# Optimization experiments

Hardware: AMD Instinct MI355X
Metric: run time of the kernel (lower is better)

## Reference

```python
import jax, jax.numpy as jnp
import numpy as np

B, T, J, C = 32, 256, 21, 3
BT = B * T
N = BT * J

_TPL_SRC = np.array([0, 1, 2, 3, 4, 0, 5, 6, 7, 8, 0, 9, 10, 11, 12, 0, 13, 14, 15, 16, 0, 17, 18, 19, 20], np.int32)
_TPL_DST = np.array([1, 2, 3, 4, 0, 5, 6, 7, 8, 0, 9, 10, 11, 12, 0, 13, 14, 15, 16, 0, 17, 18, 19, 20, 0], np.int32)


def _build_edges():
    off = (np.arange(BT, dtype=np.int32) * J)[:, None]
    src = (_TPL_SRC[None, :] + off).ravel()
    dst = (_TPL_DST[None, :] + off).ravel()
    # PyG GATConv default add_self_loops=True (both layers see the same augmented set)
    loops = np.arange(N, dtype=np.int32)
    return np.concatenate([src, loops]), np.concatenate([dst, loops])


def setup_inputs() -> dict:
    key = jax.random.key(0)
    ks = jax.random.split(key, 8)
    src, dst = _build_edges()
    return {
        "keypoints": jax.random.normal(ks[0], (B, T, J, C), jnp.float32),
        "W1": jax.random.normal(ks[1], (3, 256), jnp.float32) * 0.3,
        "att1_src": jax.random.normal(ks[2], (4, 64), jnp.float32) * 0.1,
        "att1_dst": jax.random.normal(ks[3], (4, 64), jnp.float32) * 0.1,
        "b1": jnp.zeros((256,), jnp.float32),
        "W2": jax.random.normal(ks[4], (256, 128), jnp.float32) * 0.06,
        "att2_src": jax.random.normal(ks[5], (1, 128), jnp.float32) * 0.1,
        "att2_dst": jax.random.normal(ks[6], (1, 128), jnp.float32) * 0.1,
        "b2": jnp.zeros((128,), jnp.float32),
        "src": jnp.asarray(src),
        "dst": jnp.asarray(dst),
    }


def _gat_conv(x, src, dst, W, a_src, a_dst, b, heads, d_head):
    n = x.shape[0]
    h = (x @ W).reshape(n, heads, d_head)            # [N,H,D]
    e_s = jnp.einsum('nhd,hd->nh', h, a_src)          # [N,H]
    e_d = jnp.einsum('nhd,hd->nh', h, a_dst)
    e = jax.nn.leaky_relu(e_s[src] + e_d[dst], 0.2)   # [E,H]
    m = jax.ops.segment_max(e, dst, num_segments=n)
    ex = jnp.exp(e - m[dst])
    z = jax.ops.segment_sum(ex, dst, num_segments=n)
    alpha = ex / z[dst]                               # scatter-softmax over dst
    out = jax.ops.segment_sum(h[src] * alpha[:, :, None], dst, num_segments=n)
    return out.reshape(n, heads * d_head) + b


def reference(keypoints, W1, att1_src, att1_dst, b1, W2, att2_src, att2_dst, b2, src, dst):
    x = keypoints.reshape(N, C)
    x = jax.nn.relu(_gat_conv(x, src, dst, W1, att1_src, att1_dst, b1, 4, 64))
    x = jax.nn.relu(_gat_conv(x, src, dst, W2, att2_src, att2_dst, b2, 1, 128))
    x = x.reshape(BT, J, 128).mean(axis=1)            # pool joints
    return x.reshape(B, T, 128).mean(axis=1)          # pool time -> [B,128]
```

## Files before the change

kernel.cpp:

```cpp
#include <hip/hip_runtime.h>

#define NJ  21
#define X1S 264
#define H2S 136
#define XAS 40

typedef __attribute__((ext_vector_type(8))) short  bf16x8;
typedef __attribute__((ext_vector_type(4))) float  floatx4;

__device__ __forceinline__ float lrelu(float v){ return v > 0.f ? v : 0.2f*v; }
__device__ __forceinline__ unsigned short f2bf(float x){
  unsigned int u = __float_as_uint(x);
  return (unsigned short)((u + 0x7FFFu + ((u >> 16) & 1u)) >> 16);
}
__device__ __forceinline__ float bf2f(unsigned short h){
  return __uint_as_float(((unsigned int)h) << 16);
}

__global__ void prep(const float* __restrict__ W1, const float* __restrict__ a1s,
                     const float* __restrict__ a1d, const float* __restrict__ W2,
                     unsigned short* __restrict__ w2f, unsigned short* __restrict__ w1b,
                     float* __restrict__ ws1o){
  const int t = threadIdx.x, b = blockIdx.x;
  if (b < 32){
    int base = b*1024 + t*4;
    #pragma unroll
    for (int i = 0; i < 4; ++i){
      int idx = base + i;
      int j = idx & 7, lane = (idx >> 3) & 63, nt = (idx >> 9) & 7, kt = idx >> 12;
      int k = kt*32 + (lane >> 4)*8 + j;
      int n = nt*16 + (lane & 15);
      w2f[idx] = f2bf(W2[k*128 + n]);
    }
  } else if (b < 40){
    int base = (b - 32)*1024 + t*4;
    #pragma unroll
    for (int i = 0; i < 4; ++i){
      int idx = base + i;
      int j = idx & 7, lane = (idx >> 3) & 63, nt = idx >> 9;
      int k = (lane >> 4)*8 + j;
      int n = nt*16 + (lane & 15);
      float v = 0.f;
      if (k < 16){
        int h = k >> 2, c = k & 3;
        if (c < 3 && h == (n >> 6)) v = W1[c*256 + n];
      }
      w1b[idx] = f2bf(v);
    }
  } else if (t < 24){
    int c = t % 3, h = (t/3) & 3, sd = t/12;
    const float* av = sd ? a1d : a1s;
    float s = 0.f;
    #pragma unroll
    for (int d = 0; d < 64; ++d) s += W1[c*256 + h*64 + d]*av[h*64 + d];
    ws1o[sd*12 + c*4 + h] = s;
  }
}

__global__ __launch_bounds__(256, 4)
void gat_fused(const float* __restrict__ kp,  const float* __restrict__ b1v,
               const float* __restrict__ a2s, const float* __restrict__ a2d,
               const float* __restrict__ b2v, const unsigned short* __restrict__ w2f,
               const unsigned short* __restrict__ w1b, const float* __restrict__ ws1g,
               float* __restrict__ out)
{
  __shared__ float xsL[2][NJ][4];
  __shared__ unsigned short xagb[48*XAS];
  __shared__ unsigned short x1bf[48*X1S];
  __shared__ float a2sL[128], a2dL[128];
  __shared__ float es2[42], ed2[42];
  __shared__ float al2L[42][8];
  __shared__ float pool2[128];
  unsigned short* h2bf = x1bf;

  const int t = threadIdx.x, blk = blockIdx.x;
  const int w = t >> 6, lane = t & 63, quad = lane >> 4, ln15 = lane & 15;
  const int h = t & 3;

  float wsr[3], wdr[3];
  #pragma unroll
  for (int c = 0; c < 3; ++c){ wsr[c] = ws1g[c*4 + h]; wdr[c] = ws1g[12 + c*4 + h]; }

  if (t < 126){ int f8 = t >= 63; int r = t - 63*f8; xsL[f8][r/3][r%3] = kp[blk*126 + t]; }
  if (t < 128) a2sL[t] = a2s[t]; else a2dL[t-128] = a2d[t-128];
  for (int o = t; o < 960; o += 256) ((unsigned*)xagb)[o] = 0u;
  __syncthreads();

  if (t < 168){
    int fn = t >> 2, fl = fn >= NJ, n = fn - fl*NJ;
    int p[6], np;
    if (n == 0){ p[0]=4;p[1]=8;p[2]=12;p[3]=16;p[4]=20;p[5]=0; np=6; }
    else       { p[0]=(n%4==1)?0:(n-1); p[1]=n; np=2; }
    float4 xself = *(const float4*)&xsL[fl][n][0];
    float ed = xself.x*wdr[0] + xself.y*wdr[1] + xself.z*wdr[2];
    float4 xp[6]; float e[6]; float m = -1e30f;
    for (int i = 0; i < np; ++i){
      xp[i] = *(const float4*)&xsL[fl][p[i]][0];
      float es = xp[i].x*wsr[0] + xp[i].y*wsr[1] + xp[i].z*wsr[2];
      e[i] = lrelu(es + ed); m = fmaxf(m, e[i]);
    }
    float z = 0.f;
    for (int i = 0; i < np; ++i){ e[i] = __expf(e[i]-m); z += e[i]; }
    float inv = 1.f/z;
    float a0 = 0.f, a1 = 0.f, a2v = 0.f;
    for (int i = 0; i < np; ++i){
      float al = e[i]*inv;
      a0 += al*xp[i].x; a1 += al*xp[i].y; a2v += al*xp[i].z;
    }
    uint2 pk;
    pk.x = (unsigned)f2bf(a0) | ((unsigned)f2bf(a1) << 16);
    pk.y = (unsigned)f2bf(a2v);
    *(uint2*)&xagb[fn*XAS + h*4] = pk;
  }
  __syncthreads();

  {
    bf16x8 A[3];
    #pragma unroll
    for (int mt = 0; mt < 3; ++mt)
      A[mt] = *(bf16x8*)&xagb[(mt*16 + ln15)*XAS + quad*8];
    #pragma unroll
    for (int i = 0; i < 4; ++i){
      const int cb = w*64 + i*16 + ln15;
      bf16x8 Bv = *(const bf16x8*)(w1b + (unsigned)((w*4 + i)*64 + lane)*8);
      floatx4 c0 = {0.f,0.f,0.f,0.f}, c1 = c0, c2 = c0;
      c0 = __builtin_amdgcn_mfma_f32_16x16x32_bf16(A[0], Bv, c0, 0,0,0);
      c1 = __builtin_amdgcn_mfma_f32_16x16x32_bf16(A[1], Bv, c1, 0,0,0);
      c2 = __builtin_amdgcn_mfma_f32_16x16x32_bf16(A[2], Bv, c2, 0,0,0);
      float bb = b1v[cb];
      #pragma unroll
      for (int r = 0; r < 4; ++r){
        x1bf[(     quad*4 + r)*X1S + cb] = f2bf(fmaxf(c0[r] + bb, 0.f));
        x1bf[(16 + quad*4 + r)*X1S + cb] = f2bf(fmaxf(c1[r] + bb, 0.f));
        x1bf[(32 + quad*4 + r)*X1S + cb] = f2bf(fmaxf(c2[r] + bb, 0.f));
      }
    }
  }
  __syncthreads();

  floatx4 acc[3][2];
  #pragma unroll
  for (int mt = 0; mt < 3; ++mt){ acc[mt][0] = (floatx4){0.f,0.f,0.f,0.f}; acc[mt][1] = acc[mt][0]; }
  #pragma unroll
  for (int kt = 0; kt < 8; ++kt){
    bf16x8 a0 = *(bf16x8*)&x1bf[(     ln15)*X1S + kt*32 + quad*8];
    bf16x8 a1 = *(bf16x8*)&x1bf[(16 + ln15)*X1S + kt*32 + quad*8];
    bf16x8 a2 = *(bf16x8*)&x1bf[(32 + ln15)*X1S + kt*32 + quad*8];
    bf16x8 b0 = *(const bf16x8*)(w2f + (unsigned)((kt*8 + 2*w    )*64 + lane)*8);
    bf16x8 b1 = *(const bf16x8*)(w2f + (unsigned)((kt*8 + 2*w + 1)*64 + lane)*8);
    acc[0][0] = __builtin_amdgcn_mfma_f32_16x16x32_bf16(a0, b0, acc[0][0], 0,0,0);
    acc[0][1] = __builtin_amdgcn_mfma_f32_16x16x32_bf16(a0, b1, acc[0][1], 0,0,0);
    acc[1][0] = __builtin_amdgcn_mfma_f32_16x16x32_bf16(a1, b0, acc[1][0], 0,0,0);
    acc[1][1] = __builtin_amdgcn_mfma_f32_16x16x32_bf16(a1, b1, acc[1][1], 0,0,0);
    acc[2][0] = __builtin_amdgcn_mfma_f32_16x16x32_bf16(a2, b0, acc[2][0], 0,0,0);
    acc[2][1] = __builtin_amdgcn_mfma_f32_16x16x32_bf16(a2, b1, acc[2][1], 0,0,0);
  }
  __syncthreads();
  {
    const int c0 = 32*w + ln15, c1 = c0 + 16;
    #pragma unroll
    for (int mt = 0; mt < 3; ++mt){
      #pragma unroll
      for (int r = 0; r < 4; ++r){
        int row = mt*16 + quad*4 + r;
        if (row < 42){
          h2bf[row*H2S + c0] = f2bf(acc[mt][0][r]);
          h2bf[row*H2S + c1] = f2bf(acc[mt][1][r]);
        }
      }
    }
  }
  __syncthreads();

  if (t < 168){
    int fn = t >> 2, q = t & 3;
    float s = 0.f, d = 0.f;
    #pragma unroll
    for (int jb = 0; jb < 4; ++jb){
      bf16x8 hv = *(bf16x8*)&h2bf[fn*H2S + q*32 + jb*8];
      float4 as0 = *(const float4*)&a2sL[q*32 + jb*8];
      float4 as1 = *(const float4*)&a2sL[q*32 + jb*8 + 4];
      float4 ad0 = *(const float4*)&a2dL[q*32 + jb*8];
      float4 ad1 = *(const float4*)&a2dL[q*32 + jb*8 + 4];
      float h0 = bf2f((unsigned short)hv[0]), h1 = bf2f((unsigned short)hv[1]);
      float h2v= bf2f((unsigned short)hv[2]), h3 = bf2f((unsigned short)hv[3]);
      float h4 = bf2f((unsigned short)hv[4]), h5 = bf2f((unsigned short)hv[5]);
      float h6 = bf2f((unsigned short)hv[6]), h7 = bf2f((unsigned short)hv[7]);
      s += h0*as0.x + h1*as0.y + h2v*as0.z + h3*as0.w
         + h4*as1.x + h5*as1.y + h6*as1.z  + h7*as1.w;
      d += h0*ad0.x + h1*ad0.y + h2v*ad0.z + h3*ad0.w
         + h4*ad1.x + h5*ad1.y + h6*ad1.z  + h7*ad1.w;
    }
    s += __shfl_xor(s, 1); s += __shfl_xor(s, 2);
    d += __shfl_xor(d, 1); d += __shfl_xor(d, 2);
    if (q == 0){ es2[fn] = s; ed2[fn] = d; }
  }
  __syncthreads();

  if (t < 42){
    int fl = t >= NJ, n = t - fl*NJ, base = fl*NJ;
    int p[6], np;
    if (n == 0){ p[0]=4;p[1]=8;p[2]=12;p[3]=16;p[4]=20;p[5]=0; np=6; }
    else       { p[0]=(n%4==1)?0:(n-1); p[1]=n; np=2; }
    float ed = ed2[t];
    float e[6], m = -1e30f;
    for (int i = 0; i < np; ++i){ e[i] = lrelu(es2[base + p[i]] + ed); m = fmaxf(m, e[i]); }
    float z = 0.f;
    for (int i = 0; i < np; ++i){ e[i] = __expf(e[i]-m); z += e[i]; }
    float inv = 1.f/z;
    for (int i = 0; i < np; ++i) al2L[t][i] = e[i]*inv;
  }
  __syncthreads();

  {
    int fl = t >> 7, j = t & 127, base = fl*NJ;
    float bj = b2v[j];
    float h0 = bf2f(h2bf[base*H2S + j]);
    float v0 = al2L[base][5]*h0;
    float s = 0.f, hprev = h0;
    #pragma unroll
    for (int n = 1; n < NJ; ++n){
      float hn = bf2f(h2bf[(base+n)*H2S + j]);
      float pv = ((n & 3) == 1) ? h0 : hprev;
      float2 al = *(const float2*)&al2L[base+n][0];
      s += fmaxf(bj + al.x*pv + al.y*hn, 0.f);
      if ((n & 3) == 0) v0 += al2L[base][(n >> 2) - 1]*hn;
      hprev = hn;
    }
    s += fmaxf(bj + v0, 0.f);
    if (t >= 128) pool2[j] = s;
    __syncthreads();
    if (t < 128) atomicAdd(&out[(blk >> 7)*128 + j], (s + pool2[j])*(1.f/5376.f));
  }
}

extern "C" void kernel_launch(void* const* d_in, const int* in_sizes, int n_in,
                              void* d_out, int out_size, void* d_ws, size_t ws_size,
                              hipStream_t stream){
  const float* kp  = (const float*)d_in[0];
  const float* W1  = (const float*)d_in[1];
  const float* a1s = (const float*)d_in[2];
  const float* a1d = (const float*)d_in[3];
  const float* b1  = (const float*)d_in[4];
  const float* W2  = (const float*)d_in[5];
  const float* a2s = (const float*)d_in[6];
  const float* a2d = (const float*)d_in[7];
  const float* b2  = (const float*)d_in[8];
  float* out = (float*)d_out;

  unsigned short* w2f = (unsigned short*)d_ws;
  unsigned short* w1b = (unsigned short*)((char*)d_ws + 65536);
  float* ws1 = (float*)((char*)d_ws + 65536 + 16384);

  hipMemsetAsync(out, 0, (size_t)out_size*sizeof(float), stream);
  prep<<<41, 256, 0, stream>>>(W1, a1s, a1d, W2, w2f, w1b, ws1);
  gat_fused<<<4096, 256, 0, stream>>>(kp, b1, a2s, a2d, b2, w2f, w1b, ws1, out);
}
```

Measured before the change: 134.2 us.

## Double block to 512 threads splitting MFMA work across 8 waves; fold memset into prep

The fused GAT kernel now runs with 512 threads (8 wavefronts) per block. Each wave computes half as many output columns in both MFMA GEMMs, which cuts per-thread accumulator registers and spreads the attention-logit reduction over 8 lanes per node. The separate hipMemsetAsync on the output is removed and the zeroing is done inside the prep kernel, dropping one launch. The cost is that many threads sit idle during the serial softmax and pooling phases, and the larger blocks with launch_bounds(512,8) may limit how many blocks fit per CU.

After: 158.5 us. +18.1%, slower.

```diff
diff --git a/kernel.cpp b/kernel.cpp
--- a/kernel.cpp
+++ b/kernel.cpp
@@ -20,7 +20,7 @@
 __global__ void prep(const float* __restrict__ W1, const float* __restrict__ a1s,
                      const float* __restrict__ a1d, const float* __restrict__ W2,
                      unsigned short* __restrict__ w2f, unsigned short* __restrict__ w1b,
-                     float* __restrict__ ws1o){
+                     float* __restrict__ ws1o, float* __restrict__ out){
   const int t = threadIdx.x, b = blockIdx.x;
   if (b < 32){
     int base = b*1024 + t*4;
@@ -47,17 +47,20 @@
       }
       w1b[idx] = f2bf(v);
     }
-  } else if (t < 24){
-    int c = t % 3, h = (t/3) & 3, sd = t/12;
-    const float* av = sd ? a1d : a1s;
-    float s = 0.f;
-    #pragma unroll
-    for (int d = 0; d < 64; ++d) s += W1[c*256 + h*64 + d]*av[h*64 + d];
-    ws1o[sd*12 + c*4 + h] = s;
-  }
-}
-
-__global__ __launch_bounds__(256, 4)
+  } else {
+    if (t < 24){
+      int c = t % 3, h = (t/3) & 3, sd = t/12;
+      const float* av = sd ? a1d : a1s;
+      float s = 0.f;
+      #pragma unroll
+      for (int d = 0; d < 64; ++d) s += W1[c*256 + h*64 + d]*av[h*64 + d];
+      ws1o[sd*12 + c*4 + h] = s;
+    }
+    for (int i = t; i < 4096; i += 256) out[i] = 0.f;
+  }
+}
+
+__global__ __launch_bounds__(512, 8)
 void gat_fused(const float* __restrict__ kp,  const float* __restrict__ b1v,
                const float* __restrict__ a2s, const float* __restrict__ a2d,
                const float* __restrict__ b2v, const unsigned short* __restrict__ w2f,
@@ -82,8 +85,9 @@
   for (int c = 0; c < 3; ++c){ wsr[c] = ws1g[c*4 + h]; wdr[c] = ws1g[12 + c*4 + h]; }
 
   if (t < 126){ int f8 = t >= 63; int r = t - 63*f8; xsL[f8][r/3][r%3] = kp[blk*126 + t]; }
-  if (t < 128) a2sL[t] = a2s[t]; else a2dL[t-128] = a2d[t-128];
-  for (int o = t; o < 960; o += 256) ((unsigned*)xagb)[o] = 0u;
+  if (t >= 256 && t < 384) a2sL[t-256] = a2s[t-256];
+  if (t >= 384)            a2dL[t-384] = a2d[t-384];
+  for (int o = t; o < 960; o += 512) ((unsigned*)xagb)[o] = 0u;
   __syncthreads();
 
   if (t < 168){
@@ -115,18 +119,17 @@
   __syncthreads();
 
   {
-    bf16x8 A[3];
-    #pragma unroll
-    for (int mt = 0; mt < 3; ++mt)
-      A[mt] = *(bf16x8*)&xagb[(mt*16 + ln15)*XAS + quad*8];
-    #pragma unroll
-    for (int i = 0; i < 4; ++i){
-      const int cb = w*64 + i*16 + ln15;
-      bf16x8 Bv = *(const bf16x8*)(w1b + (unsigned)((w*4 + i)*64 + lane)*8);
+    bf16x8 A0 = *(bf16x8*)&xagb[(     ln15)*XAS + quad*8];
+    bf16x8 A1 = *(bf16x8*)&xagb[(16 + ln15)*XAS + quad*8];
+    bf16x8 A2 = *(bf16x8*)&xagb[(32 + ln15)*XAS + quad*8];
+    #pragma unroll
+    for (int i = 0; i < 2; ++i){
+      const int cb = w*32 + i*16 + ln15;
+      bf16x8 Bv = *(const bf16x8*)(w1b + (unsigned)((w*2 + i)*64 + lane)*8);
       floatx4 c0 = {0.f,0.f,0.f,0.f}, c1 = c0, c2 = c0;
-      c0 = __builtin_amdgcn_mfma_f32_16x16x32_bf16(A[0], Bv, c0, 0,0,0);
-      c1 = __builtin_amdgcn_mfma_f32_16x16x32_bf16(A[1], Bv, c1, 0,0,0);
-      c2 = __builtin_amdgcn_mfma_f32_16x16x32_bf16(A[2], Bv, c2, 0,0,0);
+      c0 = __builtin_amdgcn_mfma_f32_16x16x32_bf16(A0, Bv, c0, 0,0,0);
+      c1 = __builtin_amdgcn_mfma_f32_16x16x32_bf16(A1, Bv, c1, 0,0,0);
+      c2 = __builtin_amdgcn_mfma_f32_16x16x32_bf16(A2, Bv, c2, 0,0,0);
       float bb = b1v[cb];
       #pragma unroll
       for (int r = 0; r < 4; ++r){
@@ -138,50 +141,42 @@
   }
   __syncthreads();
 
-  floatx4 acc[3][2];
-  #pragma unroll
-  for (int mt = 0; mt < 3; ++mt){ acc[mt][0] = (floatx4){0.f,0.f,0.f,0.f}; acc[mt][1] = acc[mt][0]; }
+  floatx4 acc0 = {0.f,0.f,0.f,0.f}, acc1 = acc0, acc2 = acc0;
   #pragma unroll
   for (int kt = 0; kt < 8; ++kt){
     bf16x8 a0 = *(bf16x8*)&x1bf[(     ln15)*X1S + kt*32 + quad*8];
     bf16x8 a1 = *(bf16x8*)&x1bf[(16 + ln15)*X1S + kt*32 + quad*8];
     bf16x8 a2 = *(bf16x8*)&x1bf[(32 + ln15)*X1S + kt*32 + quad*8];
-    bf16x8 b0 = *(const bf16x8*)(w2f + (unsigned)((kt*8 + 2*w    )*64 + lane)*8);
-    bf16x8 b1 = *(const bf16x8*)(w2f + (unsigned)((kt*8 + 2*w + 1)*64 + lane)*8);
-    acc[0][0] = __builtin_amdgcn_mfma_f32_16x16x32_bf16(a0, b0, acc[0][0], 0,0,0);
-    acc[0][1] = __builtin_amdgcn_mfma_f32_16x16x32_bf16(a0, b1, acc[0][1], 0,0,0);
-    acc[1][0] = __builtin_amdgcn_mfma_f32_16x16x32_bf16(a1, b0, acc[1][0], 0,0,0);
-    acc[1][1] = __builtin_amdgcn_mfma_f32_16x16x32_bf16(a1, b1, acc[1][1], 0,0,0);
-    acc[2][0] = __builtin_amdgcn_mfma_f32_16x16x32_bf16(a2, b0, acc[2][0], 0,0,0);
-    acc[2][1] = __builtin_amdgcn_mfma_f32_16x16x32_bf16(a2, b1, acc[2][1], 0,0,0);
+    bf16x8 b0 = *(const bf16x8*)(w2f + (unsigned)((kt*8 + w)*64 + lane)*8);
+    acc0 = __builtin_amdgcn_mfma_f32_16x16x32_bf16(a0, b0, acc0, 0,0,0);
+    acc1 = __builtin_amdgcn_mfma_f32_16x16x32_bf16(a1, b0, acc1, 0,0,0);
+    acc2 = __builtin_amdgcn_mfma_f32_16x16x32_bf16(a2, b0, acc2, 0,0,0);
   }
   __syncthreads();
   {
-    const int c0 = 32*w + ln15, c1 = c0 + 16;
-    #pragma unroll
-    for (int mt = 0; mt < 3; ++mt){
-      #pragma unroll
-      for (int r = 0; r < 4; ++r){
-        int row = mt*16 + quad*4 + r;
-        if (row < 42){
-          h2bf[row*H2S + c0] = f2bf(acc[mt][0][r]);
-          h2bf[row*H2S + c1] = f2bf(acc[mt][1][r]);
-        }
-      }
-    }
-  }
-  __syncthreads();
-
-  if (t < 168){
-    int fn = t >> 2, q = t & 3;
+    const int c0 = 16*w + ln15;
+    #pragma unroll
+    for (int r = 0; r < 4; ++r){
+      int row0 =      quad*4 + r;
+      int row1 = 16 + quad*4 + r;
+      int row2 = 32 + quad*4 + r;
+      h2bf[row0*H2S + c0] = f2bf(acc0[r]);
+      h2bf[row1*H2S + c0] = f2bf(acc1[r]);
+      if (row2 < 42) h2bf[row2*H2S + c0] = f2bf(acc2[r]);
+    }
+  }
+  __syncthreads();
+
+  if (t < 336){
+    int fn = t >> 3, oct = t & 7, j0 = oct*16;
     float s = 0.f, d = 0.f;
     #pragma unroll
-    for (int jb = 0; jb < 4; ++jb){
-      bf16x8 hv = *(bf16x8*)&h2bf[fn*H2S + q*32 + jb*8];
-      float4 as0 = *(const float4*)&a2sL[q*32 + jb*8];
-      float4 as1 = *(const float4*)&a2sL[q*32 + jb*8 + 4];
-      float4 ad0 = *(const float4*)&a2dL[q*32 + jb*8];
-      float4 ad1 = *(const float4*)&a2dL[q*32 + jb*8 + 4];
+    for (int jb = 0; jb < 2; ++jb){
+      bf16x8 hv = *(bf16x8*)&h2bf[fn*H2S + j0 + jb*8];
+      float4 as0 = *(const float4*)&a2sL[j0 + jb*8];
+      float4 as1 = *(const float4*)&a2sL[j0 + jb*8 + 4];
+      float4 ad0 = *(const float4*)&a2dL[j0 + jb*8];
+      float4 ad1 = *(const float4*)&a2dL[j0 + jb*8 + 4];
       float h0 = bf2f((unsigned short)hv[0]), h1 = bf2f((unsigned short)hv[1]);
       float h2v= bf2f((unsigned short)hv[2]), h3 = bf2f((unsigned short)hv[3]);
       float h4 = bf2f((unsigned short)hv[4]), h5 = bf2f((unsigned short)hv[5]);
@@ -191,9 +186,9 @@
       d += h0*ad0.x + h1*ad0.y + h2v*ad0.z + h3*ad0.w
          + h4*ad1.x + h5*ad1.y + h6*ad1.z  + h7*ad1.w;
     }
-    s += __shfl_xor(s, 1); s += __shfl_xor(s, 2);
-    d += __shfl_xor(d, 1); d += __shfl_xor(d, 2);
-    if (q == 0){ es2[fn] = s; ed2[fn] = d; }
+    s += __shfl_xor(s, 1); s += __shfl_xor(s, 2); s += __shfl_xor(s, 4);
+    d += __shfl_xor(d, 1); d += __shfl_xor(d, 2); d += __shfl_xor(d, 4);
+    if (oct == 0){ es2[fn] = s; ed2[fn] = d; }
   }
   __syncthreads();
 
@@ -212,7 +207,8 @@
   }
   __syncthreads();
 
-  {
+  float psum = 0.f;
+  if (t < 256){
     int fl = t >> 7, j = t & 127, base = fl*NJ;
     float bj = b2v[j];
     float h0 = bf2f(h2bf[base*H2S + j]);
@@ -228,10 +224,11 @@
       hprev = hn;
     }
     s += fmaxf(bj + v0, 0.f);
+    psum = s;
     if (t >= 128) pool2[j] = s;
-    __syncthreads();
-    if (t < 128) atomicAdd(&out[(blk >> 7)*128 + j], (s + pool2[j])*(1.f/5376.f));
-  }
+  }
+  __syncthreads();
+  if (t < 128) atomicAdd(&out[(blk >> 7)*128 + t], (psum + pool2[t])*(1.f/5376.f));
 }
 
 extern "C" void kernel_launch(void* const* d_in, const int* in_sizes, int n_in,
@@ -252,7 +249,6 @@
   unsigned short* w1b = (unsigned short*)((char*)d_ws + 65536);
   float* ws1 = (float*)((char*)d_ws + 65536 + 16384);
 
-  hipMemsetAsync(out, 0, (size_t)out_size*sizeof(float), stream);
-  prep<<<41, 256, 0, stream>>>(W1, a1s, a1d, W2, w2f, w1b, ws1);
-  gat_fused<<<4096, 256, 0, stream>>>(kp, b1, a2s, a2d, b2, w2f, w1b, ws1, out);
-}
+  prep<<<41, 256, 0, stream>>>(W1, a1s, a1d, W2, w2f, w1b, ws1, out);
+  gat_fused<<<4096, 512, 0, stream>>>(kp, b1, a2s, a2d, b2, w2f, w1b, ws1, out);
+}
```

## Fuse weight preprocessing into main GAT kernel and drop prep launch

Applied to the files above, without the earlier changes.

Removes the separate prep kernel. Each block now builds the layer-1 attention projections in shared memory, forms the W1 MFMA operand in registers, and converts W2 fp32 to bf16 on the fly from global memory. Shared buffers are aliased into a union and launch bounds are raised to 5 blocks per CU to improve occupancy. The cost is redundant weight conversion and 2x-larger fp32 W2 loads with strided access in every block, in exchange for dropping a kernel launch and its dependency.

Result: slower. 141.6 us (+5.5%).

```diff
diff --git a/kernel.cpp b/kernel.cpp
--- a/kernel.cpp
+++ b/kernel.cpp
@@ -13,81 +13,55 @@
   unsigned int u = __float_as_uint(x);
   return (unsigned short)((u + 0x7FFFu + ((u >> 16) & 1u)) >> 16);
 }
+__device__ __forceinline__ unsigned pk2bf(float lo, float hi){
+  unsigned a = __float_as_uint(lo) + 0x8000u;
+  unsigned b = __float_as_uint(hi) + 0x8000u;
+  return (a >> 16) | (b & 0xFFFF0000u);
+}
 __device__ __forceinline__ float bf2f(unsigned short h){
   return __uint_as_float(((unsigned int)h) << 16);
 }
 
-__global__ void prep(const float* __restrict__ W1, const float* __restrict__ a1s,
-                     const float* __restrict__ a1d, const float* __restrict__ W2,
-                     unsigned short* __restrict__ w2f, unsigned short* __restrict__ w1b,
-                     float* __restrict__ ws1o){
-  const int t = threadIdx.x, b = blockIdx.x;
-  if (b < 32){
-    int base = b*1024 + t*4;
-    #pragma unroll
-    for (int i = 0; i < 4; ++i){
-      int idx = base + i;
-      int j = idx & 7, lane = (idx >> 3) & 63, nt = (idx >> 9) & 7, kt = idx >> 12;
-      int k = kt*32 + (lane >> 4)*8 + j;
-      int n = nt*16 + (lane & 15);
-      w2f[idx] = f2bf(W2[k*128 + n]);
-    }
-  } else if (b < 40){
-    int base = (b - 32)*1024 + t*4;
-    #pragma unroll
-    for (int i = 0; i < 4; ++i){
-      int idx = base + i;
-      int j = idx & 7, lane = (idx >> 3) & 63, nt = idx >> 9;
-      int k = (lane >> 4)*8 + j;
-      int n = nt*16 + (lane & 15);
-      float v = 0.f;
-      if (k < 16){
-        int h = k >> 2, c = k & 3;
-        if (c < 3 && h == (n >> 6)) v = W1[c*256 + n];
-      }
-      w1b[idx] = f2bf(v);
-    }
-  } else if (t < 24){
-    int c = t % 3, h = (t/3) & 3, sd = t/12;
+__global__ __launch_bounds__(256, 5)
+void gat_fused(const float* __restrict__ kp,  const float* __restrict__ W1,
+               const float* __restrict__ a1s, const float* __restrict__ a1d,
+               const float* __restrict__ b1v, const float* __restrict__ W2,
+               const float* __restrict__ a2s, const float* __restrict__ a2d,
+               const float* __restrict__ b2v, float* __restrict__ out)
+{
+  __shared__ float xsL[2][NJ][4];
+  __shared__ float wsl[2][12];
+  __shared__ unsigned char uni[3840] __attribute__((aligned(16)));
+  __shared__ unsigned short x1bf[48*X1S];
+  __shared__ float a2sL[128], a2dL[128];
+  unsigned short* xagb  = (unsigned short*)uni;
+  float*          es2   = (float*)uni;
+  float*          ed2   = (float*)(uni + 176);
+  float (*al2L)[8]      = (float(*)[8])(uni + 352);
+  float*          pool2 = (float*)(uni + 1792);
+  unsigned short* h2bf  = x1bf;
+
+  const int t = threadIdx.x, blk = blockIdx.x;
+  const int w = t >> 6, lane = t & 63, quad = lane >> 4, ln15 = lane & 15;
+
+  if (t < 126){ int fl = t >= 63; int r = t - 63*fl; xsL[fl][r/3][r%3] = kp[blk*126 + t]; }
+  if (t < 128) a2sL[t] = a2s[t]; else a2dL[t-128] = a2d[t-128];
+  for (int o = t; o < 960; o += 256) ((unsigned*)xagb)[o] = 0u;
+  if (t >= 160 && t < 184){
+    int q = t - 160, c = q % 3, h = (q/3) & 3, sd = q/12;
     const float* av = sd ? a1d : a1s;
     float s = 0.f;
     #pragma unroll
     for (int d = 0; d < 64; ++d) s += W1[c*256 + h*64 + d]*av[h*64 + d];
-    ws1o[sd*12 + c*4 + h] = s;
-  }
-}
-
-__global__ __launch_bounds__(256, 4)
-void gat_fused(const float* __restrict__ kp,  const float* __restrict__ b1v,
-               const float* __restrict__ a2s, const float* __restrict__ a2d,
-               const float* __restrict__ b2v, const unsigned short* __restrict__ w2f,
-               const unsigned short* __restrict__ w1b, const float* __restrict__ ws1g,
-               float* __restrict__ out)
-{
-  __shared__ float xsL[2][NJ][4];
-  __shared__ unsigned short xagb[48*XAS];
-  __shared__ unsigned short x1bf[48*X1S];
-  __shared__ float a2sL[128], a2dL[128];
-  __shared__ float es2[42], ed2[42];
-  __shared__ float al2L[42][8];
-  __shared__ float pool2[128];
-  unsigned short* h2bf = x1bf;
-
-  const int t = threadIdx.x, blk = blockIdx.x;
-  const int w = t >> 6, lane = t & 63, quad = lane >> 4, ln15 = lane & 15;
-  const int h = t & 3;
-
-  float wsr[3], wdr[3];
-  #pragma unroll
-  for (int c = 0; c < 3; ++c){ wsr[c] = ws1g[c*4 + h]; wdr[c] = ws1g[12 + c*4 + h]; }
-
-  if (t < 126){ int f8 = t >= 63; int r = t - 63*f8; xsL[f8][r/3][r%3] = kp[blk*126 + t]; }
-  if (t < 128) a2sL[t] = a2s[t]; else a2dL[t-128] = a2d[t-128];
-  for (int o = t; o < 960; o += 256) ((unsigned*)xagb)[o] = 0u;
+    wsl[sd][c*4 + h] = s;
+  }
   __syncthreads();
 
   if (t < 168){
-    int fn = t >> 2, fl = fn >= NJ, n = fn - fl*NJ;
+    int fn = t >> 2, fl = fn >= NJ, n = fn - fl*NJ, h = t & 3;
+    float wsr[3], wdr[3];
+    #pragma unroll
+    for (int c = 0; c < 3; ++c){ wsr[c] = wsl[0][c*4+h]; wdr[c] = wsl[1][c*4+h]; }
     int p[6], np;
     if (n == 0){ p[0]=4;p[1]=8;p[2]=12;p[3]=16;p[4]=20;p[5]=0; np=6; }
     else       { p[0]=(n%4==1)?0:(n-1); p[1]=n; np=2; }
@@ -115,18 +89,24 @@
   __syncthreads();
 
   {
-    bf16x8 A[3];
-    #pragma unroll
-    for (int mt = 0; mt < 3; ++mt)
-      A[mt] = *(bf16x8*)&xagb[(mt*16 + ln15)*XAS + quad*8];
+    bf16x8 A0 = *(bf16x8*)&xagb[(     ln15)*XAS + quad*8];
+    bf16x8 A1 = *(bf16x8*)&xagb[(16 + ln15)*XAS + quad*8];
+    bf16x8 A2 = *(bf16x8*)&xagb[(32 + ln15)*XAS + quad*8];
     #pragma unroll
     for (int i = 0; i < 4; ++i){
       const int cb = w*64 + i*16 + ln15;
-      bf16x8 Bv = *(const bf16x8*)(w1b + (unsigned)((w*4 + i)*64 + lane)*8);
+      float wv0 = W1[cb], wv1 = W1[256 + cb], wv2 = W1[512 + cb];
+      bf16x8 Bv;
+      #pragma unroll
+      for (int j = 0; j < 8; ++j){
+        int hh = quad*2 + (j >> 2), c = j & 3;
+        float v = (quad < 2 && c < 3 && hh == w) ? (c == 0 ? wv0 : (c == 1 ? wv1 : wv2)) : 0.f;
+        Bv[j] = (short)f2bf(v);
+      }
       floatx4 c0 = {0.f,0.f,0.f,0.f}, c1 = c0, c2 = c0;
-      c0 = __builtin_amdgcn_mfma_f32_16x16x32_bf16(A[0], Bv, c0, 0,0,0);
-      c1 = __builtin_amdgcn_mfma_f32_16x16x32_bf16(A[1], Bv, c1, 0,0,0);
-      c2 = __builtin_amdgcn_mfma_f32_16x16x32_bf16(A[2], Bv, c2, 0,0,0);
+      c0 = __builtin_amdgcn_mfma_f32_16x16x32_bf16(A0, Bv, c0, 0,0,0);
+      c1 = __builtin_amdgcn_mfma_f32_16x16x32_bf16(A1, Bv, c1, 0,0,0);
+      c2 = __builtin_amdgcn_mfma_f32_16x16x32_bf16(A2, Bv, c2, 0,0,0);
       float bb = b1v[cb];
       #pragma unroll
       for (int r = 0; r < 4; ++r){
@@ -141,19 +121,31 @@
   floatx4 acc[3][2];
   #pragma unroll
   for (int mt = 0; mt < 3; ++mt){ acc[mt][0] = (floatx4){0.f,0.f,0.f,0.f}; acc[mt][1] = acc[mt][0]; }
-  #pragma unroll
-  for (int kt = 0; kt < 8; ++kt){
-    bf16x8 a0 = *(bf16x8*)&x1bf[(     ln15)*X1S + kt*32 + quad*8];
-    bf16x8 a1 = *(bf16x8*)&x1bf[(16 + ln15)*X1S + kt*32 + quad*8];
-    bf16x8 a2 = *(bf16x8*)&x1bf[(32 + ln15)*X1S + kt*32 + quad*8];
-    bf16x8 b0 = *(const bf16x8*)(w2f + (unsigned)((kt*8 + 2*w    )*64 + lane)*8);
-    bf16x8 b1 = *(const bf16x8*)(w2f + (unsigned)((kt*8 + 2*w + 1)*64 + lane)*8);
-    acc[0][0] = __builtin_amdgcn_mfma_f32_16x16x32_bf16(a0, b0, acc[0][0], 0,0,0);
-    acc[0][1] = __builtin_amdgcn_mfma_f32_16x16x32_bf16(a0, b1, acc[0][1], 0,0,0);
-    acc[1][0] = __builtin_amdgcn_mfma_f32_16x16x32_bf16(a1, b0, acc[1][0], 0,0,0);
-    acc[1][1] = __builtin_amdgcn_mfma_f32_16x16x32_bf16(a1, b1, acc[1][1], 0,0,0);
-    acc[2][0] = __builtin_amdgcn_mfma_f32_16x16x32_bf16(a2, b0, acc[2][0], 0,0,0);
-    acc[2][1] = __builtin_amdgcn_mfma_f32_16x16x32_bf16(a2, b1, acc[2][1], 0,0,0);
+  {
+    const int n0 = w*32 + ln15;
+    #pragma unroll
+    for (int kt = 0; kt < 8; ++kt){
+      bf16x8 a0 = *(bf16x8*)&x1bf[(     ln15)*X1S + kt*32 + quad*8];
+      bf16x8 a1 = *(bf16x8*)&x1bf[(16 + ln15)*X1S + kt*32 + quad*8];
+      bf16x8 a2 = *(bf16x8*)&x1bf[(32 + ln15)*X1S + kt*32 + quad*8];
+      const float* wp = W2 + (kt*32 + quad*8)*128;
+      bf16x8 b0, b1;
+      unsigned* b0d = (unsigned*)&b0;
+      unsigned* b1d = (unsigned*)&b1;
+      #pragma unroll
+      for (int jj = 0; jj < 4; ++jj){
+        float l0 = wp[(2*jj  )*128 + n0     ], h0 = wp[(2*jj+1)*128 + n0     ];
+        float l1 = wp[(2*jj  )*128 + n0 + 16], h1 = wp[(2*jj+1)*128 + n0 + 16];
+        b0d[jj] = pk2bf(l0, h0);
+        b1d[jj] = pk2bf(l1, h1);
+      }
+      acc[0][0] = __builtin_amdgcn_mfma_f32_16x16x32_bf16(a0, b0, acc[0][0], 0,0,0);
+      acc[0][1] = __builtin_amdgcn_mfma_f32_16x16x32_bf16(a0, b1, acc[0][1], 0,0,0);
+      acc[1][0] = __builtin_amdgcn_mfma_f32_16x16x32_bf16(a1, b0, acc[1][0], 0,0,0);
+      acc[1][1] = __builtin_amdgcn_mfma_f32_16x16x32_bf16(a1, b1, acc[1][1], 0,0,0);
+      acc[2][0] = __builtin_amdgcn_mfma_f32_16x16x32_bf16(a2, b0, acc[2][0], 0,0,0);
+      acc[2][1] = __builtin_amdgcn_mfma_f32_16x16x32_bf16(a2, b1, acc[2][1], 0,0,0);
+    }
   }
   __syncthreads();
   {
@@ -247,12 +239,6 @@
   const float* a2d = (const float*)d_in[7];
   const float* b2  = (const float*)d_in[8];
   float* out = (float*)d_out;
-
-  unsigned short* w2f = (unsigned short*)d_ws;
-  unsigned short* w1b = (unsigned short*)((char*)d_ws + 65536);
-  float* ws1 = (float*)((char*)d_ws + 65536 + 16384);
-
   hipMemsetAsync(out, 0, (size_t)out_size*sizeof(float), stream);
-  prep<<<41, 256, 0, stream>>>(W1, a1s, a1d, W2, w2f, w1b, ws1);
-  gat_fused<<<4096, 256, 0, stream>>>(kp, b1, a2s, a2d, b2, w2f, w1b, ws1, out);
-}
+  gat_fused<<<4096, 256, 0, stream>>>(kp, W1, a1s, a1d, b1, W2, a2s, a2d, b2, out);
+}
```
